# Kernel optimization log

Hardware: AMD Instinct MI355X
Metric: run time of the kernel (lower is better)

The kernel has to match this reference:

```python
import jax, jax.numpy as jnp
import numpy as np
import math

U = 1024      # units
H = 16        # num_head
DH = U // H   # units_head
B = 2
Q = 1024      # query length
M = 1024      # memory length
KL = M + Q    # key length
R = KL + 1    # relative positions length (rel-shift needs k_len+1)
EPS = 1e-7    # K.epsilon()


def setup_inputs() -> dict:
    key = jax.random.key(0)
    ks = jax.random.split(key, 11)
    f32 = jnp.float32
    return {
        "inputs": jax.random.normal(ks[0], (B, Q, U), f32),
        "content": jax.random.normal(ks[1], (B, Q, U), f32),
        "memories": jax.random.normal(ks[2], (B, M, U), f32),
        "relatives": jax.random.normal(ks[3], (B, R, U), f32),
        "segment_mat": jax.random.uniform(ks[4], (B, Q, KL, 2), f32),
        "segment_embed": jax.random.normal(ks[5], (2, U), f32) * 0.02,
        "bias_context": jax.random.normal(ks[6], (U,), f32) * 0.02,
        "bias_relative": jax.random.normal(ks[7], (U,), f32) * 0.02,
        "bias_segment": jax.random.normal(ks[8], (U,), f32) * 0.02,
        "permutation": jax.random.uniform(ks[9], (B, Q, KL), f32),
        "kernel": jax.random.normal(ks[10], (U, 5 * U), f32) * 0.02,
    }


def _heads(x):
    # [B, L, U] -> [B, H, L, DH]
    b, l, _ = x.shape
    return x.reshape(b, l, H, DH).transpose(0, 2, 1, 3)


def _rel_shift(x, klen):
    # Transformer-XL relative shift via reshape trick. x: [B, H, Q, R]
    b, h, q, r = x.shape
    x = x.reshape(b, h, r, q)[:, :, 1:, :].reshape(b, h, q, r - 1)
    return x[:, :, :, :klen]


def reference(inputs, content, memories, relatives, segment_mat, segment_embed,
              bias_context, bias_relative, bias_segment, permutation, kernel):
    k_q = kernel[:, :U]
    k_kv = kernel[:, U:3 * U]
    k_r = kernel[:, 3 * U:4 * U]
    k_o = kernel[:, 4 * U:5 * U]

    full = jnp.concatenate([memories, content], axis=1)          # [B, KL, U]
    w_q = inputs @ k_q                                           # [B, Q, U]
    w_kv = full @ k_kv                                           # [B, KL, 2U]
    w_r = relatives @ k_r                                        # [B, R, U]

    w_k = _heads(w_kv[..., :U])                                  # [B, H, KL, DH]
    w_v = _heads(w_kv[..., U:])                                  # [B, H, KL, DH]

    # content term
    q_c = _heads(w_q + bias_context)                             # [B, H, Q, DH]
    a_context = jnp.einsum('bhqd,bhkd->bhqk', q_c, w_k)

    # relative-position term with rel-shift
    q_r = _heads(w_q + bias_relative)
    w_r_h = _heads(w_r)                                          # [B, H, R, DH]
    a_relative = _rel_shift(jnp.einsum('bhqd,bhrd->bhqr', q_r, w_r_h), KL)

    # segment term
    q_s = _heads(w_q + bias_segment)                             # [B, H, Q, DH]
    seg_e = segment_embed.T.reshape(H, DH, 2)                    # [H, DH, 2]
    qs_seg = jnp.einsum('bhqd,hds->bhqs', q_s, seg_e)            # [B, H, Q, 2]
    a_segment = jnp.einsum('bqks,bhqs->bhqk', segment_mat, qs_seg)

    att = (a_context + a_relative + a_segment) / math.sqrt(DH)   # [B, H, Q, KL]
    e = jnp.exp(att - jnp.max(att, axis=-1, keepdims=True))
    e = e * permutation[:, None, :, :]
    att = e / (jnp.sum(e, axis=-1, keepdims=True) + EPS)

    out = jnp.einsum('bhqk,bhkd->bhqd', att, w_v)                # [B, H, Q, DH]
    out = out.transpose(0, 2, 1, 3).reshape(inputs.shape[0], Q, U)
    return out @ k_o                                             # [B, Q, U]
```

## Files before the change

kernel.cpp:

```cpp
#include <hip/hip_runtime.h>

typedef __bf16 bf16;
typedef unsigned short u16;
typedef unsigned int u32;
typedef __attribute__((ext_vector_type(8))) __bf16 bf16x8;
typedef __attribute__((ext_vector_type(4))) __bf16 bf16x4;
typedef __attribute__((ext_vector_type(4))) float f32x4;
typedef __attribute__((ext_vector_type(8))) float f32x8;

#define SWZ(r, s) (((r) << 3) + ((s) ^ ((r) & 7)))
#define GSW(r, s) (((r) << 2) + ((s) ^ (((r) >> 1) & 3)))

__device__ __forceinline__ f32x4 mfma16(bf16x8 a, bf16x8 b, f32x4 c) {
  return __builtin_amdgcn_mfma_f32_16x16x32_bf16(a, b, c, 0, 0, 0);
}
__device__ __forceinline__ void gld16(const void* g, void* l) {
  __builtin_amdgcn_global_load_lds((const __attribute__((address_space(1))) void*)g,
                                   (__attribute__((address_space(3))) void*)l, 16, 0, 0);
}

__global__ __launch_bounds__(256) void prep_all(
    const float* __restrict__ inputs, const float* __restrict__ mem,
    const float* __restrict__ cont, const float* __restrict__ rel,
    const float* __restrict__ K, bf16* __restrict__ in_b,
    bf16* __restrict__ full_b, bf16* __restrict__ rel_b, bf16* __restrict__ KT) {
  __shared__ float t[64][68];
  const int bid = blockIdx.x, tid = threadIdx.x;
  if (bid < 1024) {
    size_t i = ((size_t)bid * 256 + tid) * 8;
    f32x8 v = *reinterpret_cast<const f32x8*>(inputs + i);
    *reinterpret_cast<bf16x8*>(in_b + i) = __builtin_convertvector(v, bf16x8);
  } else if (bid < 3072) {
    size_t i = ((size_t)(bid - 1024) * 256 + tid) * 8;
    int row = (int)(i >> 10), col = (int)(i & 1023);
    int b = row >> 11, r = row & 2047;
    const float* src = (r < 1024)
        ? (mem  + (((size_t)(b << 10) + r)          << 10) + col)
        : (cont + (((size_t)(b << 10) + (r - 1024)) << 10) + col);
    f32x8 v = *reinterpret_cast<const f32x8*>(src);
    *reinterpret_cast<bf16x8*>(full_b + i) = __builtin_convertvector(v, bf16x8);
  } else if (bid < 5121) {
    size_t i = ((size_t)(bid - 3072) * 256 + tid) * 8;
    f32x8 v = *reinterpret_cast<const f32x8*>(rel + i);
    *reinterpret_cast<bf16x8*>(rel_b + i) = __builtin_convertvector(v, bf16x8);
  } else {
    const int r = bid - 5121;
    const int n0 = (r % 80) << 6, k0 = (r / 80) << 6;
    for (int idx = tid; idx < 1024; idx += 256) {
      int rr = idx >> 4, c4 = (idx & 15) << 2;
      f32x4 v = *reinterpret_cast<const f32x4*>(K + (size_t)(k0 + rr) * 5120 + n0 + c4);
      t[rr][c4] = v.x; t[rr][c4 + 1] = v.y; t[rr][c4 + 2] = v.z; t[rr][c4 + 3] = v.w;
    }
    __syncthreads();
    for (int idx = tid; idx < 1024; idx += 256) {
      int rr = idx >> 4, c4 = (idx & 15) << 2;
      bf16x4 o = { (bf16)t[c4][rr], (bf16)t[c4 + 1][rr], (bf16)t[c4 + 2][rr], (bf16)t[c4 + 3][rr] };
      *reinterpret_cast<bf16x4*>(KT + (size_t)(n0 + rr) * 1024 + k0 + c4) = o;
    }
  }
}

template<int MT, int OUT_MODE, int KLEN, bool KWRAP>
__device__ __forceinline__ void gemm_body(
    const bf16* __restrict__ A, const bf16* __restrict__ BT,
    void* __restrict__ C0v, void* __restrict__ C1v,
    int m0, int n0, int Mrows, int splitN, bf16* As, bf16* Bs, int tid) {
  const int l = tid & 63, w = tid >> 6;
  const int wn = (w & 1) << 6;
  const int wm = (w >> 1) * (MT / 2);
  constexpr int MFR = MT / 32;
  const int lc = l & 15, l16 = l >> 4;
  f32x4 acc[MFR][4] = {};
  const int r0 = tid >> 2;
  const int sq = tid & 3;
  const int g0 = (sq ^ ((r0 >> 1) & 3)) << 3;

  for (int k0 = 0; k0 < KLEN; k0 += 32) {
    const int kk = KWRAP ? (k0 & 1023) : k0;
    __syncthreads();
    gld16(A  + (size_t)(m0 + r0) * KLEN + k0 + g0, &As[tid << 3]);
    gld16(BT + (size_t)(n0 + r0) * 1024 + kk + g0, &Bs[tid << 3]);
    if (MT == 128)
      gld16(A + (size_t)(m0 + r0 + 64) * KLEN + k0 + g0, &As[(tid + 256) << 3]);
    gld16(BT + (size_t)(n0 + r0 + 64) * 1024 + kk + g0, &Bs[(tid + 256) << 3]);
    __syncthreads();
    bf16x8 af[MFR], bfv[4];
#pragma unroll
    for (int m = 0; m < MFR; ++m)
      af[m] = *reinterpret_cast<const bf16x8*>(&As[GSW(wm + (m << 4) + lc, l16) << 3]);
#pragma unroll
    for (int n = 0; n < 4; ++n)
      bfv[n] = *reinterpret_cast<const bf16x8*>(&Bs[GSW(wn + (n << 4) + lc, l16) << 3]);
#pragma unroll
    for (int m = 0; m < MFR; ++m)
#pragma unroll
      for (int n = 0; n < 4; ++n)
        acc[m][n] = mfma16(af[m], bfv[n], acc[m][n]);
  }
#pragma unroll
  for (int m = 0; m < MFR; ++m) {
    const int rbase = m0 + wm + (m << 4) + (l16 << 2);
#pragma unroll
    for (int n = 0; n < 4; ++n) {
      const int col = n0 + wn + (n << 4) + lc;
      const int cc = (col < splitN) ? col : (col - splitN);
      void* Cv = (col < splitN) ? C0v : C1v;
#pragma unroll
      for (int r = 0; r < 4; ++r) {
        const int row = rbase + r;
        if (row < Mrows) {
          const float v = acc[m][n][r];
          const size_t off = ((size_t)row << 10) + cc;
          if (OUT_MODE == 1) ((bf16*)Cv)[off] = (bf16)v;
          else               ((float*)Cv)[off] = v;
        }
      }
    }
  }
}

__global__ __launch_bounds__(256) void proj_fused(
    const bf16* __restrict__ in_b, const bf16* __restrict__ full_b,
    const bf16* __restrict__ rel_b, const bf16* __restrict__ kT,
    bf16* __restrict__ w_q, bf16* __restrict__ w_k, bf16* __restrict__ w_v,
    bf16* __restrict__ w_rh) {
  __shared__ bf16 As[4096];
  __shared__ bf16 Bs[4096];
  const int bid = blockIdx.x, tid = threadIdx.x;
  if (bid < 256) {
    gemm_body<64, 1, 1024, false>(in_b, kT, w_q, w_q,
                                  (bid >> 3) << 6, (bid & 7) << 7, 2048, 1 << 30, As, Bs, tid);
  } else if (bid < 768) {
    const int r = bid - 256;
    gemm_body<128, 1, 1024, false>(full_b, kT + (1 << 20), w_k, w_v,
                                   (r >> 4) << 7, (r & 15) << 7, 4096, 1024, As, Bs, tid);
  } else {
    const int r = bid - 768;
    gemm_body<64, 1, 1024, false>(rel_b, kT + 3 * (1 << 20), w_rh, w_rh,
                                  (r >> 3) << 6, (r & 7) << 7, 4098, 1 << 30, As, Bs, tid);
  }
}

__global__ __launch_bounds__(256) void out_proj(
    const bf16* __restrict__ a_cat, const bf16* __restrict__ kTo,
    float* __restrict__ out) {
  __shared__ bf16 As[4096];
  __shared__ bf16 Bs[4096];
  const int bid = blockIdx.x, tid = threadIdx.x;
  gemm_body<64, 0, 2048, true>(a_cat, kTo, out, out,
                               (bid >> 3) << 6, (bid & 7) << 7, 2048, 1 << 30, As, Bs, tid);
}

__global__ __launch_bounds__(256) void mid_prep(
    const float* __restrict__ seg_mat, bf16* __restrict__ seg_b,
    const bf16* __restrict__ w_q, const float* __restrict__ bias_s,
    const float* __restrict__ seg_embed, float* __restrict__ qs) {
  const int bid = blockIdx.x, tid = threadIdx.x;
  if (bid < 4096) {
    size_t i = ((size_t)bid * 256 + tid) * 8;
    f32x8 v = *reinterpret_cast<const f32x8*>(seg_mat + i);
    *reinterpret_cast<bf16x8*>(seg_b + i) = __builtin_convertvector(v, bf16x8);
  } else {
    int idx = (bid - 4096) * 256 + tid;
    int q = idx & 1023, h = (idx >> 10) & 15, b = idx >> 14;
    const bf16* wp = w_q + (((size_t)(b << 10) + q) << 10) + (h << 6);
    const float* bp = bias_s + (h << 6);
    const float* e0 = seg_embed + (h << 6);
    const float* e1 = seg_embed + 1024 + (h << 6);
    float s0 = 0.f, s1 = 0.f;
#pragma unroll 8
    for (int d = 0; d < 64; ++d) {
      float v = (float)wp[d] + bp[d];
      s0 = fmaf(v, e0[d], s0);
      s1 = fmaf(v, e1[d], s1);
    }
    qs[((size_t)idx << 1) + 0] = s0;
    qs[((size_t)idx << 1) + 1] = s1;
  }
}

__global__ __launch_bounds__(256) void attn_mfma(
    const bf16* __restrict__ w_q, const bf16* __restrict__ w_k,
    const bf16* __restrict__ w_v, const bf16* __restrict__ w_rh,
    const float* __restrict__ qs_seg, const bf16* __restrict__ seg_b,
    const float* __restrict__ perm, const float* __restrict__ bias_c,
    const float* __restrict__ bias_r, bf16* __restrict__ a_cat) {
  const int id = blockIdx.x;
  const int h  = (id >> 3) & 15;
  const int cg = (id & 7) | ((id >> 7) << 3);
  const int qt = cg & 15, b = cg >> 4;
  const int qi0 = qt << 6;
  const int tid = threadIdx.x;
  const int w = tid >> 6, l = tid & 63;
  const int lc = l & 15, l16 = l >> 4;
  const int w16 = w << 4;
  const int myq = w16 + lc;

  __shared__ bf16 kt[2][2048];
  __shared__ u16  vt[2][2560];
  __shared__ bf16 wbc[8192];
  __shared__ bf16 wb2[6144];
  __shared__ u16  pl[2560];
  __shared__ float ART[4 * 960];
  __shared__ float facw[64], lroww[64];

  auto stageK = [&](int buf, int kj) {
    int r = tid >> 3, s = tid & 7;
    gld16(w_k + ((size_t)((b << 11) + kj + r) << 10) + (h << 6) + ((s ^ (r & 7)) << 3),
          &kt[buf][tid << 3]);
  };
  auto stageWB = [&](int L0, int nrows, int OFF) {
    for (int base = 0; base < nrows; base += 32) {
      int r = (tid >> 3) + base, s = tid & 7;
      int L = L0 + r;
      int slot = (L + OFF) & 127;
      int grow = L > 2048 ? 2048 : L;
      gld16(w_rh + ((size_t)(b * 2049 + grow) << 10) + (h << 6) + ((s ^ (slot & 7)) << 3),
            &wbc[((slot << 3) | s) << 3]);
    }
  };
  auto stageWB2 = [&]() {
    for (int base = 0; base < 96; base += 32) {
      int r = (tid >> 3) + base, s = tid & 7;
      gld16(w_rh + ((size_t)(b * 2049 + r) << 10) + (h << 6) + ((s ^ (r & 7)) << 3),
            &wb2[((r << 3) | s) << 3]);
    }
  };
  const int kv2 = (tid & 15) << 1, d4 = ((tid >> 4) & 15) << 2, kw = tid & 15;
  auto loadV = [&](int kj, uint2& ra, uint2& rb) {
    const u16* vp = (const u16*)w_v + ((size_t)((b << 11) + kj + kv2) << 10) + (h << 6) + d4;
    ra = *reinterpret_cast<const uint2*>(vp);
    rb = *reinterpret_cast<const uint2*>(vp + 1024);
  };
  auto writeV = [&](int buf, uint2 ra, uint2 rb) {
    u32* vt32 = reinterpret_cast<u32*>(&vt[buf][0]);
    vt32[(d4 + 0) * 20 + kw] = (ra.x & 0xffffu) | (rb.x << 16);
    vt32[(d4 + 1) * 20 + kw] = (ra.x >> 16) | (rb.x & 0xffff0000u);
    vt32[(d4 + 2) * 20 + kw] = (ra.y & 0xffffu) | (rb.y << 16);
    vt32[(d4 + 3) * 20 + kw] = (ra.y >> 16) | (rb.y & 0xffff0000u);
  };
  const size_t qrowg = (size_t)((b << 10) + qi0 + myq);
  auto loadSP = [&](int kj, bf16x8& sA, bf16x8& sB, f32x4& pA, f32x4& pB) {
    const bf16* sp = seg_b + (qrowg * 2048 + kj + (l16 << 2)) * 2;
    sA = *reinterpret_cast<const bf16x8*>(sp);
    sB = *reinterpret_cast<const bf16x8*>(sp + 32);
    const float* pp = perm + qrowg * 2048 + kj + (l16 << 2);
    pA = *reinterpret_cast<const f32x4*>(pp);
    pB = *reinterpret_cast<const f32x4*>(pp + 16);
  };

  stageK(0, 0);
  stageWB(961 - qi0, 96, 7);
  uint2 ra0, rb0;
  loadV(0, ra0, rb0);
  bf16x8 segA_c, segB_c, segA_n = {}, segB_n = {};
  f32x4 pmA_c, pmB_c, pmA_n = {}, pmB_n = {};
  loadSP(0, segA_c, segB_c, pmA_c, pmB_c);

  const int dlo = l16 << 3;
  bf16x8 qcf0, qcf1, qrf0, qrf1, qrg0, qrg1;
  {
    const bf16* qb  = w_q + ((qrowg) << 10) + (h << 6);
    const int rq1 = (qi0 + myq + 1 > 1023) ? 1023 : qi0 + myq + 1;
    const bf16* qb1 = w_q + (((size_t)(b << 10) + rq1) << 10) + (h << 6);
    f32x8 bc0 = *reinterpret_cast<const f32x8*>(bias_c + (h << 6) + dlo);
    f32x8 bc1 = *reinterpret_cast<const f32x8*>(bias_c + (h << 6) + 32 + dlo);
    f32x8 br0 = *reinterpret_cast<const f32x8*>(bias_r + (h << 6) + dlo);
    f32x8 br1 = *reinterpret_cast<const f32x8*>(bias_r + (h << 6) + 32 + dlo);
    bf16x8 q0 = *reinterpret_cast<const bf16x8*>(qb + dlo);
    bf16x8 q1 = *reinterpret_cast<const bf16x8*>(qb + 32 + dlo);
    bf16x8 p0 = *reinterpret_cast<const bf16x8*>(qb1 + dlo);
    bf16x8 p1 = *reinterpret_cast<const bf16x8*>(qb1 + 32 + dlo);
    qcf0 = __builtin_convertvector(__builtin_convertvector(q0, f32x8) + bc0, bf16x8);
    qcf1 = __builtin_convertvector(__builtin_convertvector(q1, f32x8) + bc1, bf16x8);
    qrf0 = __builtin_convertvector(__builtin_convertvector(q0, f32x8) + br0, bf16x8);
    qrf1 = __builtin_convertvector(__builtin_convertvector(q1, f32x8) + br1, bf16x8);
    qrg0 = __builtin_convertvector(__builtin_convertvector(p0, f32x8) + br0, bf16x8);
    qrg1 = __builtin_convertvector(__builtin_convertvector(p1, f32x8) + br1, bf16x8);
  }
  const float* qp = qs_seg + ((((size_t)((b << 4) + h) << 10) + qi0 + myq) << 1);
  const float qs0 = qp[0], qs1 = qp[1];

  writeV(0, ra0, rb0);
  __syncthreads();

  float mrow = -1e30f, lrow = 0.f;
  f32x4 o[4] = {};
  const float SCL = 0.125f * 1.44269504f;
  int cur = 0;
  uint2 ra_n = {}, rb_n = {};

  for (int t = 0; t < 64; ++t) {
    const int kj = t << 5;
    const int rel0 = kj - qi0;
    const bool strad = (rel0 == 1024) | (rel0 == 1056);
    const bool mainB = (rel0 >= 1088);
    const int nxt = cur ^ 1;

    if (t < 63) {
      const int kjn = kj + 32, rel0n = rel0 + 32;
      stageK(nxt, kjn);
      if (rel0n == 1024) stageWB2();
      if (rel0n == 1120)      stageWB(32, 96, 0);
      else if (rel0n != 1088) {
        if (rel0n <= 1056) stageWB(rel0n + 1025, 32, 7);
        else               stageWB(rel0n - 1024, 32, 0);
      }
      loadV(kjn, ra_n, rb_n);
      loadSP(kjn, segA_n, segB_n, pmA_n, pmB_n);
    }

    f32x4 s0 = {0.f, 0.f, 0.f, 0.f}, s1 = {0.f, 0.f, 0.f, 0.f};
    {
      const bf16* ktc = kt[cur];
      bf16x8 a0 = *reinterpret_cast<const bf16x8*>(&ktc[SWZ(lc, l16) << 3]);
      bf16x8 a1 = *reinterpret_cast<const bf16x8*>(&ktc[SWZ(lc, l16 + 4) << 3]);
      bf16x8 a2 = *reinterpret_cast<const bf16x8*>(&ktc[SWZ(16 + lc, l16) << 3]);
      bf16x8 a3 = *reinterpret_cast<const bf16x8*>(&ktc[SWZ(16 + lc, l16 + 4) << 3]);
      s0 = mfma16(a0, qcf0, s0); s0 = mfma16(a1, qcf1, s0);
      s1 = mfma16(a2, qcf0, s1); s1 = mfma16(a3, qcf1, s1);
    }

    float relv[8];
    {
      const bf16x8 ar0 = mainB ? qrg0 : qrf0;
      const bf16x8 ar1 = mainB ? qrg1 : qrf1;
      const bool useWb2 = (rel0 == 1088);
      int sbase;
      if (!mainB)       sbase = (rel0 + 1016 - w16) & 127;
      else if (useWb2)  sbase = 48 - w16;
      else              sbase = (rel0 - 1040 - w16) & 127;
      const bf16* wbp = useWb2 ? wb2 : wbc;
#pragma unroll
      for (int bg = 0; bg < 3; ++bg) {
        int prow = sbase + (bg << 4) + lc;
        if (!useWb2) prow &= 127;
        bf16x8 w0 = *reinterpret_cast<const bf16x8*>(&wbp[SWZ(prow, l16) << 3]);
        bf16x8 w1 = *reinterpret_cast<const bf16x8*>(&wbp[SWZ(prow, l16 + 4) << 3]);
        f32x4 a_ = {0.f, 0.f, 0.f, 0.f};
        a_ = mfma16(ar0, w0, a_); a_ = mfma16(ar1, w1, a_);
        *reinterpret_cast<f32x4*>(&ART[w * 960 + ((bg << 4) + lc) * 20 + (l16 << 2)]) = a_;
      }
#pragma unroll
      for (int jj = 0; jj < 4; ++jj) {
        relv[jj]     = ART[w * 960 + (15 + (l16 << 2) + jj - lc) * 20 + lc];
        relv[4 + jj] = ART[w * 960 + (31 + (l16 << 2) + jj - lc) * 20 + lc];
      }
      if (strad) {
#pragma unroll
        for (int bg = 0; bg < 3; ++bg) {
          int srow = rel0 - 1040 - w16 + (bg << 4) + lc;
          srow = srow < 0 ? 0 : (srow > 95 ? 95 : srow);
          bf16x8 w0 = *reinterpret_cast<const bf16x8*>(&wb2[SWZ(srow, l16) << 3]);
          bf16x8 w1 = *reinterpret_cast<const bf16x8*>(&wb2[SWZ(srow, l16 + 4) << 3]);
          f32x4 a_ = {0.f, 0.f, 0.f, 0.f};
          a_ = mfma16(qrg0, w0, a_); a_ = mfma16(qrg1, w1, a_);
          *reinterpret_cast<f32x4*>(&ART[w * 960 + ((bg << 4) + lc) * 20 + (l16 << 2)]) = a_;
        }
#pragma unroll
        for (int jj = 0; jj < 4; ++jj) {
          const int jA = (l16 << 2) + jj, jB = 16 + jA;
          float rbA = ART[w * 960 + (15 + jA - lc) * 20 + lc];
          float rbB = ART[w * 960 + (15 + jB - lc) * 20 + lc];
          if (rel0 + jA - myq >= 1025) relv[jj] = rbA;
          if (rel0 + jB - myq >= 1025) relv[4 + jj] = rbB;
        }
      }
    }

    {
      f32x8 sgA = __builtin_convertvector(segA_c, f32x8);
      f32x8 sgB = __builtin_convertvector(segB_c, f32x8);
      float sv[8];
#pragma unroll
      for (int jj = 0; jj < 4; ++jj) {
        sv[jj]     = (s0[jj] + relv[jj]     + sgA[2 * jj] * qs0 + sgA[2 * jj + 1] * qs1) * SCL;
        sv[4 + jj] = (s1[jj] + relv[4 + jj] + sgB[2 * jj] * qs0 + sgB[2 * jj + 1] * qs1) * SCL;
      }
      float tm = sv[0];
#pragma unroll
      for (int jj = 1; jj < 8; ++jj) tm = fmaxf(tm, sv[jj]);
      tm = fmaxf(tm, __shfl_xor(tm, 16));
      tm = fmaxf(tm, __shfl_xor(tm, 32));
      const float mn2 = fmaxf(mrow, tm);
      const float facr = exp2f(mrow - mn2);
      float e[8], rs = 0.f;
#pragma unroll
      for (int jj = 0; jj < 4; ++jj) {
        e[jj]     = exp2f(sv[jj] - mn2) * pmA_c[jj];
        e[4 + jj] = exp2f(sv[4 + jj] - mn2) * pmB_c[jj];
        rs += e[jj] + e[4 + jj];
      }
      rs += __shfl_xor(rs, 16);
      rs += __shfl_xor(rs, 32);
      mrow = mn2;
      lrow = lrow * facr + rs;
      bf16x4 pa, pb;
#pragma unroll
      for (int jj = 0; jj < 4; ++jj) { pa[jj] = (bf16)e[jj]; pb[jj] = (bf16)e[4 + jj]; }
      *reinterpret_cast<bf16x4*>(&pl[myq * 40 + (l16 << 2)]) = pa;
      *reinterpret_cast<bf16x4*>(&pl[myq * 40 + 16 + (l16 << 2)]) = pb;
      if (l16 == 0) facw[myq] = facr;
    }

    {
      float fr[4];
#pragma unroll
      for (int r = 0; r < 4; ++r) fr[r] = facw[w16 + (l16 << 2) + r];
#pragma unroll
      for (int n = 0; n < 4; ++n)
#pragma unroll
        for (int r = 0; r < 4; ++r) o[n][r] *= fr[r];
      bf16x8 ap = *reinterpret_cast<const bf16x8*>(&pl[(w16 + lc) * 40 + (l16 << 3)]);
      bf16x8 bv0 = *reinterpret_cast<const bf16x8*>(&vt[cur][(lc) * 40 + (l16 << 3)]);
      bf16x8 bv1 = *reinterpret_cast<const bf16x8*>(&vt[cur][(16 + lc) * 40 + (l16 << 3)]);
      bf16x8 bv2 = *reinterpret_cast<const bf16x8*>(&vt[cur][(32 + lc) * 40 + (l16 << 3)]);
      bf16x8 bv3 = *reinterpret_cast<const bf16x8*>(&vt[cur][(48 + lc) * 40 + (l16 << 3)]);
      o[0] = mfma16(ap, bv0, o[0]);
      o[1] = mfma16(ap, bv1, o[1]);
      o[2] = mfma16(ap, bv2, o[2]);
      o[3] = mfma16(ap, bv3, o[3]);
    }

    if (t < 63) {
      writeV(nxt, ra_n, rb_n);
      segA_c = segA_n; segB_c = segB_n; pmA_c = pmA_n; pmB_c = pmB_n;
    }
    __syncthreads();
    cur = nxt;
  }

  if (l16 == 0) lroww[myq] = lrow;
  {
    float inv[4];
#pragma unroll
    for (int r = 0; r < 4; ++r)
      inv[r] = 1.f / (lroww[w16 + (l16 << 2) + r] + 1e-7f);
#pragma unroll
    for (int n = 0; n < 4; ++n) {
#pragma unroll
      for (int r = 0; r < 4; ++r) {
        const int row = qi0 + w16 + (l16 << 2) + r;
        const float v = o[n][r] * inv[r];
        const bf16 hi = (bf16)v;
        const float lof = v - (float)hi;
        const size_t off = (((size_t)(b << 10) + row) << 11) + (h << 6) + (n << 4) + lc;
        a_cat[off] = hi;
        a_cat[off + 1024] = (bf16)lof;
      }
    }
  }
}

extern "C" void kernel_launch(void* const* d_in, const int* in_sizes, int n_in,
                              void* d_out, int out_size, void* d_ws, size_t ws_size,
                              hipStream_t stream) {
  (void)in_sizes; (void)n_in; (void)out_size; (void)ws_size;
  const float* inputs    = (const float*)d_in[0];
  const float* content   = (const float*)d_in[1];
  const float* memories  = (const float*)d_in[2];
  const float* relatives = (const float*)d_in[3];
  const float* seg_mat   = (const float*)d_in[4];
  const float* seg_embed = (const float*)d_in[5];
  const float* bias_c    = (const float*)d_in[6];
  const float* bias_r    = (const float*)d_in[7];
  const float* bias_s    = (const float*)d_in[8];
  const float* perm      = (const float*)d_in[9];
  const float* kern      = (const float*)d_in[10];
  float* out = (float*)d_out;

  char* ws = (char*)d_ws;
  bf16*  in_b   = (bf16*)(ws);
  bf16*  full_b = (bf16*)(ws + 4194304);
  bf16*  rel_b  = (bf16*)(ws + 12582912);
  bf16*  kT     = (bf16*)(ws + 21233664);
  bf16*  w_q    = (bf16*)(ws + 31719424);
  bf16*  w_k    = (bf16*)(ws + 35913728);
  bf16*  w_v    = (bf16*)(ws + 44302336);
  bf16*  w_rh   = (bf16*)(ws + 52690944);
  float* qs     = (float*)(ws + 65277952);
  bf16*  seg_b  = (bf16*)(ws);
  bf16*  a_cat  = (bf16*)(ws + 21233664);
  bf16*  kTo    = (bf16*)(ws + 29622272);

  dim3 blk(256);
  prep_all<<<6401, blk, 0, stream>>>(inputs, memories, content, relatives, kern,
                                     in_b, full_b, rel_b, kT);
  proj_fused<<<1288, blk, 0, stream>>>(in_b, full_b, rel_b, kT, w_q, w_k, w_v, w_rh);
  mid_prep<<<4224, blk, 0, stream>>>(seg_mat, seg_b, w_q, bias_s, seg_embed, qs);
  attn_mfma<<<512, blk, 0, stream>>>(w_q, w_k, w_v, w_rh, qs, seg_b, perm,
                                     bias_c, bias_r, a_cat);
  out_proj<<<256, blk, 0, stream>>>(a_cat, kTo, out);
}
```

Measured before the change: 250.4 us.

## Fuse fp32-to-bf16 activation casts into projection GEMM and segment dot into attention

The projection GEMM now reads fp32 activations directly, converting them to bf16 in registers before storing to LDS, so the separate cast pass for inputs/memories/content/relatives is gone. The segment query projection (qs) is computed inside the attention kernel with a wave shuffle reduction, removing the mid_prep kernel. The seg_mat cast moves into the prep kernel, and out_proj gets its own inlined GEMM body. This cuts a launch and several MB of intermediate traffic, but the A-operand loads are now synchronous register loads instead of direct global-to-LDS copies, which may expose latency in the GEMM.

Result: faster. 244.8 us (median of 2 runs) (-2.2%).

```diff
diff --git a/kernel.cpp b/kernel.cpp
--- a/kernel.cpp
+++ b/kernel.cpp
@@ -20,32 +20,12 @@
 }
 
 __global__ __launch_bounds__(256) void prep_all(
-    const float* __restrict__ inputs, const float* __restrict__ mem,
-    const float* __restrict__ cont, const float* __restrict__ rel,
-    const float* __restrict__ K, bf16* __restrict__ in_b,
-    bf16* __restrict__ full_b, bf16* __restrict__ rel_b, bf16* __restrict__ KT) {
+    const float* __restrict__ K, const float* __restrict__ seg_mat,
+    bf16* __restrict__ KT, bf16* __restrict__ seg_b) {
   __shared__ float t[64][68];
   const int bid = blockIdx.x, tid = threadIdx.x;
-  if (bid < 1024) {
-    size_t i = ((size_t)bid * 256 + tid) * 8;
-    f32x8 v = *reinterpret_cast<const f32x8*>(inputs + i);
-    *reinterpret_cast<bf16x8*>(in_b + i) = __builtin_convertvector(v, bf16x8);
-  } else if (bid < 3072) {
-    size_t i = ((size_t)(bid - 1024) * 256 + tid) * 8;
-    int row = (int)(i >> 10), col = (int)(i & 1023);
-    int b = row >> 11, r = row & 2047;
-    const float* src = (r < 1024)
-        ? (mem  + (((size_t)(b << 10) + r)          << 10) + col)
-        : (cont + (((size_t)(b << 10) + (r - 1024)) << 10) + col);
-    f32x8 v = *reinterpret_cast<const f32x8*>(src);
-    *reinterpret_cast<bf16x8*>(full_b + i) = __builtin_convertvector(v, bf16x8);
-  } else if (bid < 5121) {
-    size_t i = ((size_t)(bid - 3072) * 256 + tid) * 8;
-    f32x8 v = *reinterpret_cast<const f32x8*>(rel + i);
-    *reinterpret_cast<bf16x8*>(rel_b + i) = __builtin_convertvector(v, bf16x8);
-  } else {
-    const int r = bid - 5121;
-    const int n0 = (r % 80) << 6, k0 = (r / 80) << 6;
+  if (bid < 1280) {
+    const int n0 = (bid % 80) << 6, k0 = (bid / 80) << 6;
     for (int idx = tid; idx < 1024; idx += 256) {
       int rr = idx >> 4, c4 = (idx & 15) << 2;
       f32x4 v = *reinterpret_cast<const f32x4*>(K + (size_t)(k0 + rr) * 5120 + n0 + c4);
@@ -57,13 +37,17 @@
       bf16x4 o = { (bf16)t[c4][rr], (bf16)t[c4 + 1][rr], (bf16)t[c4 + 2][rr], (bf16)t[c4 + 3][rr] };
       *reinterpret_cast<bf16x4*>(KT + (size_t)(n0 + rr) * 1024 + k0 + c4) = o;
     }
-  }
-}
-
-template<int MT, int OUT_MODE, int KLEN, bool KWRAP>
-__device__ __forceinline__ void gemm_body(
-    const bf16* __restrict__ A, const bf16* __restrict__ BT,
-    void* __restrict__ C0v, void* __restrict__ C1v,
+  } else {
+    size_t i = ((size_t)(bid - 1280) * 256 + tid) * 8;
+    f32x8 v = *reinterpret_cast<const f32x8*>(seg_mat + i);
+    *reinterpret_cast<bf16x8*>(seg_b + i) = __builtin_convertvector(v, bf16x8);
+  }
+}
+
+template<int MT, int AMODE>
+__device__ __forceinline__ void gemm_f32a(
+    const float* __restrict__ A1, const float* __restrict__ A2,
+    const bf16* __restrict__ BT, bf16* __restrict__ C0, bf16* __restrict__ C1,
     int m0, int n0, int Mrows, int splitN, bf16* As, bf16* Bs, int tid) {
   const int l = tid & 63, w = tid >> 6;
   const int wn = (w & 1) << 6;
@@ -75,14 +59,31 @@
   const int sq = tid & 3;
   const int g0 = (sq ^ ((r0 >> 1) & 3)) << 3;
 
-  for (int k0 = 0; k0 < KLEN; k0 += 32) {
-    const int kk = KWRAP ? (k0 & 1023) : k0;
+  auto arow = [&](int row) -> const float* {
+    if (AMODE == 0) return A1 + ((size_t)row << 10);
+    if (AMODE == 1) {
+      int b = row >> 11, rr = row & 2047;
+      return (rr < 1024) ? (A1 + (((size_t)(b << 10) + rr) << 10))
+                         : (A2 + (((size_t)(b << 10) + (rr - 1024)) << 10));
+    }
+    int rr = row > 4097 ? 4097 : row;
+    return A1 + ((size_t)rr << 10);
+  };
+  const float* ap0 = arow(m0 + r0);
+  const float* ap1 = (MT == 128) ? arow(m0 + r0 + 64) : nullptr;
+  const int aslot0 = ((r0 << 2) + (sq ^ ((r0 >> 1) & 3))) << 3;
+  const int aslot1 = (((r0 + 64) << 2) + (sq ^ ((r0 >> 1) & 3))) << 3;
+
+  for (int k0 = 0; k0 < 1024; k0 += 32) {
+    f32x8 a0 = *reinterpret_cast<const f32x8*>(ap0 + k0 + (sq << 3));
+    f32x8 a1v = {};
+    if (MT == 128) a1v = *reinterpret_cast<const f32x8*>(ap1 + k0 + (sq << 3));
     __syncthreads();
-    gld16(A  + (size_t)(m0 + r0) * KLEN + k0 + g0, &As[tid << 3]);
-    gld16(BT + (size_t)(n0 + r0) * 1024 + kk + g0, &Bs[tid << 3]);
+    *reinterpret_cast<bf16x8*>(&As[aslot0]) = __builtin_convertvector(a0, bf16x8);
     if (MT == 128)
-      gld16(A + (size_t)(m0 + r0 + 64) * KLEN + k0 + g0, &As[(tid + 256) << 3]);
-    gld16(BT + (size_t)(n0 + r0 + 64) * 1024 + kk + g0, &Bs[(tid + 256) << 3]);
+      *reinterpret_cast<bf16x8*>(&As[aslot1]) = __builtin_convertvector(a1v, bf16x8);
+    gld16(BT + (size_t)(n0 + r0) * 1024 + k0 + g0, &Bs[tid << 3]);
+    gld16(BT + (size_t)(n0 + r0 + 64) * 1024 + k0 + g0, &Bs[(tid + 256) << 3]);
     __syncthreads();
     bf16x8 af[MFR], bfv[4];
 #pragma unroll
@@ -104,40 +105,35 @@
     for (int n = 0; n < 4; ++n) {
       const int col = n0 + wn + (n << 4) + lc;
       const int cc = (col < splitN) ? col : (col - splitN);
-      void* Cv = (col < splitN) ? C0v : C1v;
+      bf16* Cv = (col < splitN) ? C0 : C1;
 #pragma unroll
       for (int r = 0; r < 4; ++r) {
         const int row = rbase + r;
-        if (row < Mrows) {
-          const float v = acc[m][n][r];
-          const size_t off = ((size_t)row << 10) + cc;
-          if (OUT_MODE == 1) ((bf16*)Cv)[off] = (bf16)v;
-          else               ((float*)Cv)[off] = v;
-        }
+        if (row < Mrows) Cv[((size_t)row << 10) + cc] = (bf16)acc[m][n][r];
       }
     }
   }
 }
 
 __global__ __launch_bounds__(256) void proj_fused(
-    const bf16* __restrict__ in_b, const bf16* __restrict__ full_b,
-    const bf16* __restrict__ rel_b, const bf16* __restrict__ kT,
-    bf16* __restrict__ w_q, bf16* __restrict__ w_k, bf16* __restrict__ w_v,
-    bf16* __restrict__ w_rh) {
+    const float* __restrict__ inputs, const float* __restrict__ mem,
+    const float* __restrict__ cont, const float* __restrict__ rel,
+    const bf16* __restrict__ kT, bf16* __restrict__ w_q, bf16* __restrict__ w_k,
+    bf16* __restrict__ w_v, bf16* __restrict__ w_rh) {
   __shared__ bf16 As[4096];
   __shared__ bf16 Bs[4096];
   const int bid = blockIdx.x, tid = threadIdx.x;
   if (bid < 256) {
-    gemm_body<64, 1, 1024, false>(in_b, kT, w_q, w_q,
-                                  (bid >> 3) << 6, (bid & 7) << 7, 2048, 1 << 30, As, Bs, tid);
+    gemm_f32a<64, 0>(inputs, nullptr, kT, w_q, w_q,
+                     (bid >> 3) << 6, (bid & 7) << 7, 2048, 1 << 30, As, Bs, tid);
   } else if (bid < 768) {
     const int r = bid - 256;
-    gemm_body<128, 1, 1024, false>(full_b, kT + (1 << 20), w_k, w_v,
-                                   (r >> 4) << 7, (r & 15) << 7, 4096, 1024, As, Bs, tid);
+    gemm_f32a<128, 1>(mem, cont, kT + (1 << 20), w_k, w_v,
+                      (r >> 4) << 7, (r & 15) << 7, 4096, 1024, As, Bs, tid);
   } else {
     const int r = bid - 768;
-    gemm_body<64, 1, 1024, false>(rel_b, kT + 3 * (1 << 20), w_rh, w_rh,
-                                  (r >> 3) << 6, (r & 7) << 7, 4098, 1 << 30, As, Bs, tid);
+    gemm_f32a<64, 2>(rel, nullptr, kT + 3 * (1 << 20), w_rh, w_rh,
+                     (r >> 3) << 6, (r & 7) << 7, 4098, 1 << 30, As, Bs, tid);
   }
 }
 
@@ -147,44 +143,56 @@
   __shared__ bf16 As[4096];
   __shared__ bf16 Bs[4096];
   const int bid = blockIdx.x, tid = threadIdx.x;
-  gemm_body<64, 0, 2048, true>(a_cat, kTo, out, out,
-                               (bid >> 3) << 6, (bid & 7) << 7, 2048, 1 << 30, As, Bs, tid);
-}
-
-__global__ __launch_bounds__(256) void mid_prep(
-    const float* __restrict__ seg_mat, bf16* __restrict__ seg_b,
-    const bf16* __restrict__ w_q, const float* __restrict__ bias_s,
-    const float* __restrict__ seg_embed, float* __restrict__ qs) {
-  const int bid = blockIdx.x, tid = threadIdx.x;
-  if (bid < 4096) {
-    size_t i = ((size_t)bid * 256 + tid) * 8;
-    f32x8 v = *reinterpret_cast<const f32x8*>(seg_mat + i);
-    *reinterpret_cast<bf16x8*>(seg_b + i) = __builtin_convertvector(v, bf16x8);
-  } else {
-    int idx = (bid - 4096) * 256 + tid;
-    int q = idx & 1023, h = (idx >> 10) & 15, b = idx >> 14;
-    const bf16* wp = w_q + (((size_t)(b << 10) + q) << 10) + (h << 6);
-    const float* bp = bias_s + (h << 6);
-    const float* e0 = seg_embed + (h << 6);
-    const float* e1 = seg_embed + 1024 + (h << 6);
-    float s0 = 0.f, s1 = 0.f;
-#pragma unroll 8
-    for (int d = 0; d < 64; ++d) {
-      float v = (float)wp[d] + bp[d];
-      s0 = fmaf(v, e0[d], s0);
-      s1 = fmaf(v, e1[d], s1);
-    }
-    qs[((size_t)idx << 1) + 0] = s0;
-    qs[((size_t)idx << 1) + 1] = s1;
+  const int m0 = (bid >> 3) << 6, n0 = (bid & 7) << 7;
+  const int l = tid & 63, w = tid >> 6;
+  const int wn = (w & 1) << 6;
+  const int wm = (w >> 1) << 5;
+  const int lc = l & 15, l16 = l >> 4;
+  f32x4 acc[2][4] = {};
+  const int r0 = tid >> 2;
+  const int sq = tid & 3;
+  const int g0 = (sq ^ ((r0 >> 1) & 3)) << 3;
+
+  for (int k0 = 0; k0 < 2048; k0 += 32) {
+    const int kk = k0 & 1023;
+    __syncthreads();
+    gld16(a_cat + (size_t)(m0 + r0) * 2048 + k0 + g0, &As[tid << 3]);
+    gld16(kTo + (size_t)(n0 + r0) * 1024 + kk + g0, &Bs[tid << 3]);
+    gld16(kTo + (size_t)(n0 + r0 + 64) * 1024 + kk + g0, &Bs[(tid + 256) << 3]);
+    __syncthreads();
+    bf16x8 af[2], bfv[4];
+#pragma unroll
+    for (int m = 0; m < 2; ++m)
+      af[m] = *reinterpret_cast<const bf16x8*>(&As[GSW(wm + (m << 4) + lc, l16) << 3]);
+#pragma unroll
+    for (int n = 0; n < 4; ++n)
+      bfv[n] = *reinterpret_cast<const bf16x8*>(&Bs[GSW(wn + (n << 4) + lc, l16) << 3]);
+#pragma unroll
+    for (int m = 0; m < 2; ++m)
+#pragma unroll
+      for (int n = 0; n < 4; ++n)
+        acc[m][n] = mfma16(af[m], bfv[n], acc[m][n]);
+  }
+#pragma unroll
+  for (int m = 0; m < 2; ++m) {
+    const int rbase = m0 + wm + (m << 4) + (l16 << 2);
+#pragma unroll
+    for (int n = 0; n < 4; ++n) {
+      const int col = n0 + wn + (n << 4) + lc;
+#pragma unroll
+      for (int r = 0; r < 4; ++r)
+        out[((size_t)(rbase + r) << 10) + col] = acc[m][n][r];
+    }
   }
 }
 
 __global__ __launch_bounds__(256) void attn_mfma(
     const bf16* __restrict__ w_q, const bf16* __restrict__ w_k,
     const bf16* __restrict__ w_v, const bf16* __restrict__ w_rh,
-    const float* __restrict__ qs_seg, const bf16* __restrict__ seg_b,
-    const float* __restrict__ perm, const float* __restrict__ bias_c,
-    const float* __restrict__ bias_r, bf16* __restrict__ a_cat) {
+    const bf16* __restrict__ seg_b, const float* __restrict__ perm,
+    const float* __restrict__ bias_c, const float* __restrict__ bias_r,
+    const float* __restrict__ bias_s, const float* __restrict__ seg_embed,
+    bf16* __restrict__ a_cat) {
   const int id = blockIdx.x;
   const int h  = (id >> 3) & 15;
   const int cg = (id & 7) | ((id >> 7) << 3);
@@ -259,6 +267,7 @@
 
   const int dlo = l16 << 3;
   bf16x8 qcf0, qcf1, qrf0, qrf1, qrg0, qrg1;
+  float qs0, qs1;
   {
     const bf16* qb  = w_q + ((qrowg) << 10) + (h << 6);
     const int rq1 = (qi0 + myq + 1 > 1023) ? 1023 : qi0 + myq + 1;
@@ -271,15 +280,31 @@
     bf16x8 q1 = *reinterpret_cast<const bf16x8*>(qb + 32 + dlo);
     bf16x8 p0 = *reinterpret_cast<const bf16x8*>(qb1 + dlo);
     bf16x8 p1 = *reinterpret_cast<const bf16x8*>(qb1 + 32 + dlo);
-    qcf0 = __builtin_convertvector(__builtin_convertvector(q0, f32x8) + bc0, bf16x8);
-    qcf1 = __builtin_convertvector(__builtin_convertvector(q1, f32x8) + bc1, bf16x8);
-    qrf0 = __builtin_convertvector(__builtin_convertvector(q0, f32x8) + br0, bf16x8);
-    qrf1 = __builtin_convertvector(__builtin_convertvector(q1, f32x8) + br1, bf16x8);
+    f32x8 qf0 = __builtin_convertvector(q0, f32x8);
+    f32x8 qf1 = __builtin_convertvector(q1, f32x8);
+    qcf0 = __builtin_convertvector(qf0 + bc0, bf16x8);
+    qcf1 = __builtin_convertvector(qf1 + bc1, bf16x8);
+    qrf0 = __builtin_convertvector(qf0 + br0, bf16x8);
+    qrf1 = __builtin_convertvector(qf1 + br1, bf16x8);
     qrg0 = __builtin_convertvector(__builtin_convertvector(p0, f32x8) + br0, bf16x8);
     qrg1 = __builtin_convertvector(__builtin_convertvector(p1, f32x8) + br1, bf16x8);
-  }
-  const float* qp = qs_seg + ((((size_t)((b << 4) + h) << 10) + qi0 + myq) << 1);
-  const float qs0 = qp[0], qs1 = qp[1];
+    f32x8 bs0 = *reinterpret_cast<const f32x8*>(bias_s + (h << 6) + dlo);
+    f32x8 bs1 = *reinterpret_cast<const f32x8*>(bias_s + (h << 6) + 32 + dlo);
+    f32x8 e00 = *reinterpret_cast<const f32x8*>(seg_embed + (h << 6) + dlo);
+    f32x8 e01 = *reinterpret_cast<const f32x8*>(seg_embed + (h << 6) + 32 + dlo);
+    f32x8 e10 = *reinterpret_cast<const f32x8*>(seg_embed + 1024 + (h << 6) + dlo);
+    f32x8 e11 = *reinterpret_cast<const f32x8*>(seg_embed + 1024 + (h << 6) + 32 + dlo);
+    f32x8 qa = qf0 + bs0, qb2 = qf1 + bs1;
+    float t0 = 0.f, t1 = 0.f;
+#pragma unroll
+    for (int j = 0; j < 8; ++j) {
+      t0 = fmaf(qa[j], e00[j], fmaf(qb2[j], e01[j], t0));
+      t1 = fmaf(qa[j], e10[j], fmaf(qb2[j], e11[j], t1));
+    }
+    t0 += __shfl_xor(t0, 16); t0 += __shfl_xor(t0, 32);
+    t1 += __shfl_xor(t1, 16); t1 += __shfl_xor(t1, 32);
+    qs0 = t0; qs1 = t1;
+  }
 
   writeV(0, ra0, rb0);
   __syncthreads();
@@ -470,25 +495,20 @@
   float* out = (float*)d_out;
 
   char* ws = (char*)d_ws;
-  bf16*  in_b   = (bf16*)(ws);
-  bf16*  full_b = (bf16*)(ws + 4194304);
-  bf16*  rel_b  = (bf16*)(ws + 12582912);
+  bf16*  seg_b  = (bf16*)(ws);
   bf16*  kT     = (bf16*)(ws + 21233664);
   bf16*  w_q    = (bf16*)(ws + 31719424);
   bf16*  w_k    = (bf16*)(ws + 35913728);
   bf16*  w_v    = (bf16*)(ws + 44302336);
   bf16*  w_rh   = (bf16*)(ws + 52690944);
-  float* qs     = (float*)(ws + 65277952);
-  bf16*  seg_b  = (bf16*)(ws);
   bf16*  a_cat  = (bf16*)(ws + 21233664);
   bf16*  kTo    = (bf16*)(ws + 29622272);
 
   dim3 blk(256);
-  prep_all<<<6401, blk, 0, stream>>>(inputs, memories, content, relatives, kern,
-                                     in_b, full_b, rel_b, kT);
-  proj_fused<<<1288, blk, 0, stream>>>(in_b, full_b, rel_b, kT, w_q, w_k, w_v, w_rh);
-  mid_prep<<<4224, blk, 0, stream>>>(seg_mat, seg_b, w_q, bias_s, seg_embed, qs);
-  attn_mfma<<<512, blk, 0, stream>>>(w_q, w_k, w_v, w_rh, qs, seg_b, perm,
-                                     bias_c, bias_r, a_cat);
+  prep_all<<<5376, blk, 0, stream>>>(kern, seg_mat, kT, seg_b);
+  proj_fused<<<1288, blk, 0, stream>>>(inputs, memories, content, relatives, kT,
+                                       w_q, w_k, w_v, w_rh);
+  attn_mfma<<<512, blk, 0, stream>>>(w_q, w_k, w_v, w_rh, seg_b, perm,
+                                     bias_c, bias_r, bias_s, seg_embed, a_cat);
   out_proj<<<256, blk, 0, stream>>>(a_cat, kTo, out);
 }
```
